# Performance work log

Measured on AMD Instinct MI355X. Metric: run time of the kernel, lower is better.

The kernel has to match this reference:

```python
import jax, jax.numpy as jnp
import numpy as np

D_MODEL = 1024
N_HEADS = 8
D_HEAD = 128
N_EXPERTS = 8
MOE_K = 2
SHARED = 1
ROUTED_E = N_EXPERTS - SHARED            # experts eligible for top-k routing
ROUTED_K = max(1, MOE_K - SHARED)        # routed slots per (token, head)
B, S = 4, 2048


def setup_inputs() -> dict:
    key = jax.random.key(0)
    ks = jax.random.split(key, 9)
    s = 1.0 / np.sqrt(D_MODEL)
    return {
        'q_src': jax.random.normal(ks[0], (B, S, D_MODEL), jnp.float32),
        'k_src': jax.random.normal(ks[1], (B, S, D_MODEL), jnp.float32),
        'v_src': jax.random.normal(ks[2], (B, S, D_MODEL), jnp.float32),
        'Wq': jax.random.normal(ks[3], (N_HEADS * D_HEAD, D_MODEL), jnp.float32) * s,
        'Wk': jax.random.normal(ks[4], (N_HEADS * D_HEAD, D_MODEL), jnp.float32) * s,
        'V': jax.random.normal(ks[5], (N_HEADS * N_EXPERTS, D_MODEL, D_HEAD), jnp.float32) * s,
        'O': jax.random.normal(ks[6], (N_HEADS * N_EXPERTS, D_HEAD, D_MODEL), jnp.float32) * (1.0 / np.sqrt(N_HEADS * D_HEAD)),
        'sel_v': jax.random.normal(ks[7], (N_HEADS * N_EXPERTS, D_MODEL), jnp.float32) * s,
        'sel_o': jax.random.normal(ks[8], (N_HEADS * N_EXPERTS, D_MODEL), jnp.float32) * s,
    }


def _gate(x, sel_w):
    # x: [B,S,D] -> sparse sigmoid gate [B,S,H,E] (eval mode: no expert dropout,
    # bias_v/bias_o are zeros so they do not change the top-k in the original).
    logits = jnp.einsum('bsd,ed->bse', x, sel_w)
    g = jax.nn.sigmoid(logits.astype(jnp.float32)).reshape(x.shape[0], x.shape[1], N_HEADS, N_EXPERTS)
    _, idx = jax.lax.top_k(g[..., :ROUTED_E], ROUTED_K)              # [B,S,H,Kr]
    shared = jnp.broadcast_to(jnp.arange(ROUTED_E, N_EXPERTS), idx.shape[:-1] + (SHARED,))
    idx = jnp.concatenate([idx, shared], axis=-1)                     # [B,S,H,K]
    vals = jnp.take_along_axis(g, idx, axis=-1)                       # sigmoid gate values
    onehot = jax.nn.one_hot(idx, N_EXPERTS, dtype=g.dtype)            # [B,S,H,K,E]
    return jnp.einsum('bshk,bshke->bshe', vals, onehot)               # sparse dense gate


def reference(q_src, k_src, v_src, Wq, Wk, V, O, sel_v, sel_o):
    scale_sqrt = jnp.asarray(D_HEAD, jnp.float32) ** -0.25  # sqrt(1/sqrt(d_head)), applied to q AND k
    b, s, _ = q_src.shape
    q = (q_src @ Wq.T * scale_sqrt).reshape(b, s, N_HEADS, D_HEAD).transpose(0, 2, 1, 3)  # [B,H,S,Dh]
    k = (k_src @ Wk.T * scale_sqrt).reshape(b, s, N_HEADS, D_HEAD).transpose(0, 2, 1, 3)

    gv = _gate(k_src, sel_v)   # value-expert gate, computed from k_src
    go = _gate(q_src, sel_o)   # output-expert gate, computed from q_src

    Vw = V.reshape(N_HEADS, N_EXPERTS, D_MODEL, D_HEAD)
    Ow = O.reshape(N_HEADS, N_EXPERTS, D_HEAD, D_MODEL)

    # CVMM value projection: per (token, head) mixture of expert V matrices
    v = jnp.einsum('bsd,hedf,bshe->bhsf', v_src, Vw, gv)              # [B,H,S,Dh]

    # SDPA, scale already folded into q and k; mask=None path
    attn = jax.nn.softmax(jnp.einsum('bhqf,bhkf->bhqk', q, k), axis=-1)
    res = jnp.einsum('bhqk,bhkf->bqhf', attn, v)                      # [B,S,H,Dh]

    # CVMM output projection: per (token, head) mixture of expert O matrices, summed over heads
    out = jnp.einsum('bqhf,hefd,bqhe->bqd', res, Ow, go)              # [B,S,D]
    return out
```

## Files before the change

kernel.cpp:

```cpp
#include <hip/hip_runtime.h>
#include <hip/hip_bf16.h>
#include <math.h>

#define BB 4
#define SS 2048
#define DM 1024
#define NH 8
#define DH 128
#define NE 8
#define NTOK (BB*SS)
#define SCALE_SQRT 0.29730177875068026f

typedef unsigned short u16;
typedef short s8v __attribute__((ext_vector_type(8)));
typedef float f4v __attribute__((ext_vector_type(4)));
#define MFMA16(a,b,c) __builtin_amdgcn_mfma_f32_16x16x32_bf16((a),(b),(c),0,0,0)

__device__ inline void bfsplit(float x, u16& h, u16& l) {
    unsigned u = __float_as_uint(x);
    unsigned hr = (u + 0x7FFFu + ((u >> 16) & 1u)) >> 16;
    h = (u16)hr;
    float hf = __uint_as_float(hr << 16);
    unsigned u2 = __float_as_uint(x - hf);
    l = (u16)((u2 + 0x7FFFu + ((u2 >> 16) & 1u)) >> 16);
}
__device__ inline u16 bf16rne(float x) {
    unsigned u = __float_as_uint(x);
    return (u16)((u + 0x7FFFu + ((u >> 16) & 1u)) >> 16);
}

__device__ inline void gll16(const u16* g, u16* l) {
    __builtin_amdgcn_global_load_lds(
        (const __attribute__((address_space(1))) unsigned int*)g,
        (__attribute__((address_space(3))) unsigned int*)l,
        16, 0, 0);
}

__device__ inline int swzoff(int row, int kchunk) {
    return row * 64 + ((kchunk ^ (row & 7)) << 3);
}

__global__ __launch_bounds__(256, 2) void proj_mfma_kernel(
        const u16* __restrict__ Ah_g, const u16* __restrict__ Al_g,
        const u16* __restrict__ Bh_g, const u16* __restrict__ Bl_g,
        u16* __restrict__ out_h, u16* __restrict__ out_l, float scale) {
    const int i0 = blockIdx.x * 128;
    const int n0 = blockIdx.y * 128;
    __shared__ u16 Ah[128 * 64], Al[128 * 64], Bh[128 * 64], Bl[128 * 64];
    const int t = threadIdx.x;
    const int lane = t & 63, wave = t >> 6;
    const int wm = wave >> 1, wn = wave & 1;
    const int ln = lane & 15, qd = lane >> 4;
    const f4v z4 = {0.f, 0.f, 0.f, 0.f};

    f4v C[4][4];
#pragma unroll
    for (int fm = 0; fm < 4; ++fm)
#pragma unroll
        for (int fn = 0; fn < 4; ++fn) C[fm][fn] = z4;

    for (int kb = 0; kb < 16; ++kb) {
        __syncthreads();
        const int kbase = kb * 64;
#pragma unroll
        for (int p = 0; p < 4; ++p) {
            int chunk = p * 256 + t;
            int row = chunk >> 3;
            int cs  = ((chunk & 7) ^ (row & 7)) * 8;
            int ld  = (p * 256 + (t & 192)) * 8;
            size_t ga = (size_t)(i0 + row) * 1024 + kbase + cs;
            gll16(&Ah_g[ga], &Ah[ld]);
            gll16(&Al_g[ga], &Al[ld]);
            size_t gb = (size_t)(n0 + row) * 1024 + kbase + cs;
            gll16(&Bh_g[gb], &Bh[ld]);
            gll16(&Bl_g[gb], &Bl[ld]);
        }
        __syncthreads();
#pragma unroll
        for (int ks = 0; ks < 2; ++ks) {
            s8v ah[4], alv[4], bh[4], blv[4];
#pragma unroll
            for (int fm = 0; fm < 4; ++fm) {
                int o = swzoff(wm * 64 + fm * 16 + ln, ks * 4 + qd);
                ah[fm]  = *(const s8v*)&Ah[o];
                alv[fm] = *(const s8v*)&Al[o];
            }
#pragma unroll
            for (int fn = 0; fn < 4; ++fn) {
                int o = swzoff(wn * 64 + fn * 16 + ln, ks * 4 + qd);
                bh[fn]  = *(const s8v*)&Bh[o];
                blv[fn] = *(const s8v*)&Bl[o];
            }
#pragma unroll
            for (int fm = 0; fm < 4; ++fm)
#pragma unroll
                for (int fn = 0; fn < 4; ++fn) {
                    C[fm][fn] = MFMA16(ah[fm],  bh[fn],  C[fm][fn]);
                    C[fm][fn] = MFMA16(ah[fm],  blv[fn], C[fm][fn]);
                    C[fm][fn] = MFMA16(alv[fm], bh[fn],  C[fm][fn]);
                }
        }
    }
    const int h = n0 >> 7;
#pragma unroll
    for (int fm = 0; fm < 4; ++fm)
#pragma unroll
        for (int fn = 0; fn < 4; ++fn)
#pragma unroll
            for (int r = 0; r < 4; ++r) {
                int token = i0 + wm * 64 + fm * 16 + qd * 4 + r;
                int f = wn * 64 + fn * 16 + ln;
                int b = token >> 11, s = token & 2047;
                u16 hh, ll;
                bfsplit(C[fm][fn][r] * scale, hh, ll);
                size_t o = ((((size_t)(b * NH + h)) * SS + s) << 7) + f;
                out_h[o] = hh; out_l[o] = ll;
            }
}

__global__ void gate_kernel(const float* __restrict__ x,
                            const float* __restrict__ sel,
                            float* __restrict__ gdense) {
    __shared__ float xs[DM];
    __shared__ float logits[64];
    __shared__ int   sbest[NH];
    __shared__ float sg1[NH], sg2[NH];
    const int token = blockIdx.x;
    const int t = threadIdx.x;
    const float* xp = x + (size_t)token * DM;
    for (int i = t; i < DM; i += 64) xs[i] = xp[i];
    __syncthreads();
    const float* sp = sel + (size_t)t * DM;
    float acc = 0.f;
    for (int d = 0; d < DM; ++d) acc += xs[d] * sp[d];
    logits[t] = acc;
    __syncthreads();
    if (t < NH) {
        const float* lp = logits + t * NE;
        int best = 0; float bv = lp[0];
#pragma unroll
        for (int e = 1; e < NE - 1; ++e)
            if (lp[e] > bv) { bv = lp[e]; best = e; }
        sbest[t] = best;
        sg1[t] = 1.f / (1.f + expf(-bv));
        sg2[t] = 1.f / (1.f + expf(-lp[NE - 1]));
    }
    __syncthreads();
    const int h = t >> 3, e = t & 7;
    float val = (e == sbest[h]) ? sg1[h] : ((e == NE - 1) ? sg2[h] : 0.f);
    gdense[(size_t)token * 64 + t] = val;
}

__global__ void split_kernel(const float* __restrict__ src,
                             u16* __restrict__ dh, u16* __restrict__ dl) {
    int i = (blockIdx.x * 256 + threadIdx.x) * 4;
    float4 v = *(const float4*)(src + i);
    u16 h[4], l[4];
    bfsplit(v.x, h[0], l[0]); bfsplit(v.y, h[1], l[1]);
    bfsplit(v.z, h[2], l[2]); bfsplit(v.w, h[3], l[3]);
    uint2 ph = { (unsigned)h[0] | ((unsigned)h[1] << 16),
                 (unsigned)h[2] | ((unsigned)h[3] << 16) };
    uint2 pl = { (unsigned)l[0] | ((unsigned)l[1] << 16),
                 (unsigned)l[2] | ((unsigned)l[3] << 16) };
    *(uint2*)&dh[i] = ph;
    *(uint2*)&dl[i] = pl;
}

__global__ void tsplit_kernel(const float* __restrict__ src,
                              u16* __restrict__ dh, u16* __restrict__ dl,
                              int R, int C) {
    __shared__ float tile[32][33];
    const int mat = blockIdx.x;
    const int r0 = blockIdx.y * 32, c0 = blockIdx.z * 32;
    const size_t base = (size_t)mat * R * C;
    const int tr = threadIdx.x >> 5, tc = threadIdx.x & 31;
#pragma unroll
    for (int p = 0; p < 4; ++p)
        tile[tr + p * 8][tc] = src[base + (size_t)(r0 + tr + p * 8) * C + c0 + tc];
    __syncthreads();
#pragma unroll
    for (int p = 0; p < 4; ++p) {
        int cc = tr + p * 8, rr = tc;
        float x = tile[rr][cc];
        u16 hh, ll; bfsplit(x, hh, ll);
        size_t o = base + (size_t)(c0 + cc) * R + r0 + rr;
        dh[o] = hh; dl[o] = ll;
    }
}

__global__ __launch_bounds__(256, 2) void v_mfma_kernel(
        const u16* __restrict__ Ah_g, const u16* __restrict__ Al_g,
        const u16* __restrict__ Bh_g, const u16* __restrict__ Bl_g,
        const float* __restrict__ gdense,
        float* __restrict__ wv) {
    const int i0 = blockIdx.x * 128;
    const int h  = blockIdx.y;
    __shared__ u16 Ah[128 * 64], Al[128 * 64], Bh[128 * 64], Bl[128 * 64];
    __shared__ float gl[128 * 8];
    const int t = threadIdx.x;
    const int lane = t & 63, wave = t >> 6;
    const int wm = wave >> 1, wn = wave & 1;
    const int ln = lane & 15, qd = lane >> 4;
    const f4v z4 = {0.f, 0.f, 0.f, 0.f};

#pragma unroll
    for (int p = 0; p < 4; ++p) {
        int idx = p * 256 + t;
        gl[idx] = gdense[(size_t)(i0 + (idx >> 3)) * 64 + h * 8 + (idx & 7)];
    }

    f4v C[4][4];
#pragma unroll
    for (int fm = 0; fm < 4; ++fm)
#pragma unroll
        for (int fn = 0; fn < 4; ++fn) C[fm][fn] = z4;

    for (int e = 0; e < 8; ++e) {
        f4v T[4][4];
#pragma unroll
        for (int fm = 0; fm < 4; ++fm)
#pragma unroll
            for (int fn = 0; fn < 4; ++fn) T[fm][fn] = z4;
        const size_t bbase = (size_t)(h * 8 + e) * DH * 1024;
        for (int kb = 0; kb < 16; ++kb) {
            __syncthreads();
            const int kbase = kb * 64;
#pragma unroll
            for (int p = 0; p < 4; ++p) {
                int chunk = p * 256 + t;
                int row = chunk >> 3;
                int cs  = ((chunk & 7) ^ (row & 7)) * 8;
                int ld  = (p * 256 + (t & 192)) * 8;
                size_t ga = (size_t)(i0 + row) * 1024 + kbase + cs;
                gll16(&Ah_g[ga], &Ah[ld]);
                gll16(&Al_g[ga], &Al[ld]);
                size_t gb = bbase + (size_t)row * 1024 + kbase + cs;
                gll16(&Bh_g[gb], &Bh[ld]);
                gll16(&Bl_g[gb], &Bl[ld]);
            }
            __syncthreads();
#pragma unroll
            for (int ks = 0; ks < 2; ++ks) {
                s8v ah[4], alv[4], bh[4], blv[4];
#pragma unroll
                for (int fm = 0; fm < 4; ++fm) {
                    int o = swzoff(wm * 64 + fm * 16 + ln, ks * 4 + qd);
                    ah[fm]  = *(const s8v*)&Ah[o];
                    alv[fm] = *(const s8v*)&Al[o];
                }
#pragma unroll
                for (int fn = 0; fn < 4; ++fn) {
                    int o = swzoff(wn * 64 + fn * 16 + ln, ks * 4 + qd);
                    bh[fn]  = *(const s8v*)&Bh[o];
                    blv[fn] = *(const s8v*)&Bl[o];
                }
#pragma unroll
                for (int fm = 0; fm < 4; ++fm)
#pragma unroll
                    for (int fn = 0; fn < 4; ++fn) {
                        T[fm][fn] = MFMA16(ah[fm],  bh[fn],  T[fm][fn]);
                        T[fm][fn] = MFMA16(ah[fm],  blv[fn], T[fm][fn]);
                        T[fm][fn] = MFMA16(alv[fm], bh[fn],  T[fm][fn]);
                    }
            }
        }
#pragma unroll
        for (int fm = 0; fm < 4; ++fm)
#pragma unroll
            for (int r = 0; r < 4; ++r) {
                float g = gl[(wm * 64 + fm * 16 + qd * 4 + r) * 8 + e];
#pragma unroll
                for (int fn = 0; fn < 4; ++fn)
                    C[fm][fn][r] += g * T[fm][fn][r];
            }
    }
#pragma unroll
    for (int fm = 0; fm < 4; ++fm)
#pragma unroll
        for (int fn = 0; fn < 4; ++fn)
#pragma unroll
            for (int r = 0; r < 4; ++r) {
                int token = i0 + wm * 64 + fm * 16 + qd * 4 + r;
                int f = wn * 64 + fn * 16 + ln;
                int b = token >> 11, s = token & 2047;
                wv[(((size_t)(b * NH + h) * SS + s) << 7) + f] = C[fm][fn][r];
            }
}

__global__ __launch_bounds__(256, 2) void out_mfma_kernel(
        const u16* __restrict__ Ah_g, const u16* __restrict__ Al_g,
        const u16* __restrict__ Bh_g, const u16* __restrict__ Bl_g,
        const float* __restrict__ gdense,
        float* __restrict__ out) {
    const int n0 = blockIdx.x * 128;
    const int i0 = blockIdx.y * 128;
    __shared__ u16 Ah[128 * 64], Al[128 * 64], Bh[128 * 64], Bl[128 * 64];
    __shared__ float gl[128 * 8];
    const int t = threadIdx.x;
    const int lane = t & 63, wave = t >> 6;
    const int wm = wave >> 1, wn = wave & 1;
    const int ln = lane & 15, qd = lane >> 4;
    const f4v z4 = {0.f, 0.f, 0.f, 0.f};

    f4v C[4][4];
#pragma unroll
    for (int fm = 0; fm < 4; ++fm)
#pragma unroll
        for (int fn = 0; fn < 4; ++fn) C[fm][fn] = z4;

    for (int h = 0; h < 8; ++h) {
        __syncthreads();
#pragma unroll
        for (int p = 0; p < 4; ++p) {
            int idx = p * 256 + t;
            gl[idx] = gdense[(size_t)(i0 + (idx >> 3)) * 64 + h * 8 + (idx & 7)];
        }
        for (int e = 0; e < 8; ++e) {
            f4v T[4][4];
#pragma unroll
            for (int fm = 0; fm < 4; ++fm)
#pragma unroll
                for (int fn = 0; fn < 4; ++fn) T[fm][fn] = z4;
            const size_t bbase = ((size_t)(h * 8 + e) * 1024 + n0) * DH;
#pragma unroll
            for (int kb = 0; kb < 2; ++kb) {
                __syncthreads();
                const int ka = h * 128 + kb * 64;
                const int kbb = kb * 64;
#pragma unroll
                for (int p = 0; p < 4; ++p) {
                    int chunk = p * 256 + t;
                    int row = chunk >> 3;
                    int cs  = ((chunk & 7) ^ (row & 7)) * 8;
                    int ld  = (p * 256 + (t & 192)) * 8;
                    size_t ga = (size_t)(i0 + row) * 1024 + ka + cs;
                    gll16(&Ah_g[ga], &Ah[ld]);
                    gll16(&Al_g[ga], &Al[ld]);
                    size_t gb = bbase + (size_t)row * DH + kbb + cs;
                    gll16(&Bh_g[gb], &Bh[ld]);
                    gll16(&Bl_g[gb], &Bl[ld]);
                }
                __syncthreads();
#pragma unroll
                for (int ks = 0; ks < 2; ++ks) {
                    s8v ah[4], alv[4], bh[4], blv[4];
#pragma unroll
                    for (int fm = 0; fm < 4; ++fm) {
                        int o = swzoff(wm * 64 + fm * 16 + ln, ks * 4 + qd);
                        ah[fm]  = *(const s8v*)&Ah[o];
                        alv[fm] = *(const s8v*)&Al[o];
                    }
#pragma unroll
                    for (int fn = 0; fn < 4; ++fn) {
                        int o = swzoff(wn * 64 + fn * 16 + ln, ks * 4 + qd);
                        bh[fn]  = *(const s8v*)&Bh[o];
                        blv[fn] = *(const s8v*)&Bl[o];
                    }
#pragma unroll
                    for (int fm = 0; fm < 4; ++fm)
#pragma unroll
                        for (int fn = 0; fn < 4; ++fn) {
                            T[fm][fn] = MFMA16(ah[fm],  bh[fn],  T[fm][fn]);
                            T[fm][fn] = MFMA16(ah[fm],  blv[fn], T[fm][fn]);
                            T[fm][fn] = MFMA16(alv[fm], bh[fn],  T[fm][fn]);
                        }
                }
            }
#pragma unroll
            for (int fm = 0; fm < 4; ++fm)
#pragma unroll
                for (int r = 0; r < 4; ++r) {
                    float g = gl[(wm * 64 + fm * 16 + qd * 4 + r) * 8 + e];
#pragma unroll
                    for (int fn = 0; fn < 4; ++fn)
                        C[fm][fn][r] += g * T[fm][fn][r];
                }
        }
    }
#pragma unroll
    for (int fm = 0; fm < 4; ++fm)
#pragma unroll
        for (int fn = 0; fn < 4; ++fn)
#pragma unroll
            for (int r = 0; r < 4; ++r) {
                int token = i0 + wm * 64 + fm * 16 + qd * 4 + r;
                int d = n0 + wn * 64 + fn * 16 + ln;
                out[(size_t)token * DM + d] = C[fm][fn][r];
            }
}

__global__ __launch_bounds__(256, 2) void attn_mfma_kernel(
        const u16* __restrict__ qh, const u16* __restrict__ ql,
        const u16* __restrict__ kh, const u16* __restrict__ kl,
        const u16* __restrict__ vth, const u16* __restrict__ vtl,
        u16* __restrict__ res_hi, u16* __restrict__ res_lo) {
    const int bid = blockIdx.x;
    const int bh = bid >> 4;
    const int q0 = (bid & 15) * 128;

    __shared__ u16 Ksh[32 * 136];
    __shared__ u16 Ksl[32 * 136];
    __shared__ u16 Vsh[128 * 40];
    __shared__ u16 Vsl[128 * 40];
    __shared__ u16 Ps[4][32 * 40];

    const int t = threadIdx.x;
    const int lane = t & 63, w = t >> 6;
    const int ln = lane & 15, qd = lane >> 4;

    s8v Qh[2][4], Qlv[2][4];
#pragma unroll
    for (int fm = 0; fm < 2; ++fm) {
        const size_t qoff = ((size_t)bh * SS + q0 + w * 32 + fm * 16 + ln) * DH;
        const u16* qhp = qh + qoff;
        const u16* qlp = ql + qoff;
#pragma unroll
        for (int ks = 0; ks < 4; ++ks) {
            Qh[fm][ks]  = *(const s8v*)(qhp + ks * 32 + qd * 8);
            Qlv[fm][ks] = *(const s8v*)(qlp + ks * 32 + qd * 8);
        }
    }

    f4v Of[2][8];
    const f4v z4 = {0.f, 0.f, 0.f, 0.f};
#pragma unroll
    for (int fm = 0; fm < 2; ++fm)
#pragma unroll
        for (int fn = 0; fn < 8; ++fn) Of[fm][fn] = z4;
    float mrow[2][4], lrow[2][4];
#pragma unroll
    for (int fm = 0; fm < 2; ++fm)
#pragma unroll
        for (int r = 0; r < 4; ++r) { mrow[fm][r] = -INFINITY; lrow[fm][r] = 0.f; }

    const u16* kbh = kh + (size_t)bh * SS * DH;
    const u16* kbl = kl + (size_t)bh * SS * DH;
    const u16* vbh = vth + (size_t)bh * DH * SS;
    const u16* vbl = vtl + (size_t)bh * DH * SS;

    const int krow0 = t >> 4,        kc0 = t & 15;
    const int krow1 = (256 + t) >> 4, kc1 = (256 + t) & 15;
    const int vrow0 = t >> 2,        vc0 = t & 3;
    const int vrow1 = (256 + t) >> 2, vc1 = (256 + t) & 3;
    const int kld0 = krow0 * 136 + kc0 * 8, kld1 = krow1 * 136 + kc1 * 8;
    const int vld0 = vrow0 * 40 + vc0 * 8,  vld1 = vrow1 * 40 + vc1 * 8;

    uint4 rKh0, rKh1, rKl0, rKl1, rVh0, rVh1, rVl0, rVl1;

#define LOADREGS(KT)                                                         \
    {                                                                        \
        size_t g0 = (size_t)((KT) * 32 + krow0) * DH + kc0 * 8;              \
        size_t g1 = (size_t)((KT) * 32 + krow1) * DH + kc1 * 8;              \
        rKh0 = *(const uint4*)&kbh[g0];  rKl0 = *(const uint4*)&kbl[g0];     \
        rKh1 = *(const uint4*)&kbh[g1];  rKl1 = *(const uint4*)&kbl[g1];     \
        size_t v0 = (size_t)vrow0 * SS + (KT) * 32 + vc0 * 8;                \
        size_t v1 = (size_t)vrow1 * SS + (KT) * 32 + vc1 * 8;                \
        rVh0 = *(const uint4*)&vbh[v0];  rVl0 = *(const uint4*)&vbl[v0];     \
        rVh1 = *(const uint4*)&vbh[v1];  rVl1 = *(const uint4*)&vbl[v1];     \
    }

#define STORELDS()                                                           \
    {                                                                        \
        *(uint4*)&Ksh[kld0] = rKh0;  *(uint4*)&Ksl[kld0] = rKl0;             \
        *(uint4*)&Ksh[kld1] = rKh1;  *(uint4*)&Ksl[kld1] = rKl1;             \
        *(uint4*)&Vsh[vld0] = rVh0;  *(uint4*)&Vsl[vld0] = rVl0;             \
        *(uint4*)&Vsh[vld1] = rVh1;  *(uint4*)&Vsl[vld1] = rVl1;             \
    }

    LOADREGS(0);
    STORELDS();
    __syncthreads();

    for (int kt = 0; kt < SS / 32; ++kt) {
        const bool more = (kt + 1 < SS / 32);
        if (more) LOADREGS(kt + 1);

        f4v S[2][2];
#pragma unroll
        for (int fm = 0; fm < 2; ++fm)
#pragma unroll
            for (int nt = 0; nt < 2; ++nt) S[fm][nt] = z4;
#pragma unroll
        for (int ks = 0; ks < 4; ++ks) {
#pragma unroll
            for (int nt = 0; nt < 2; ++nt) {
                int o = (nt * 16 + ln) * 136 + ks * 32 + qd * 8;
                s8v kbhf = *(const s8v*)&Ksh[o];
                s8v kblf = *(const s8v*)&Ksl[o];
#pragma unroll
                for (int fm = 0; fm < 2; ++fm) {
                    S[fm][nt] = MFMA16(Qh[fm][ks],  kbhf, S[fm][nt]);
                    S[fm][nt] = MFMA16(Qh[fm][ks],  kblf, S[fm][nt]);
                    S[fm][nt] = MFMA16(Qlv[fm][ks], kbhf, S[fm][nt]);
                }
            }
        }

        float pv[2][2][4];
#pragma unroll
        for (int fm = 0; fm < 2; ++fm) {
            float mt[4];
#pragma unroll
            for (int r = 0; r < 4; ++r) mt[r] = fmaxf(S[fm][0][r], S[fm][1][r]);
#pragma unroll
            for (int mask = 1; mask < 16; mask <<= 1)
#pragma unroll
                for (int r = 0; r < 4; ++r)
                    mt[r] = fmaxf(mt[r], __shfl_xor(mt[r], mask, 64));
            float alpha[4];
#pragma unroll
            for (int r = 0; r < 4; ++r) {
                float mn = fmaxf(mrow[fm][r], mt[r]);
                alpha[r] = __expf(mrow[fm][r] - mn);
                mrow[fm][r] = mn;
            }
            float lt[4] = {0.f, 0.f, 0.f, 0.f};
#pragma unroll
            for (int nt = 0; nt < 2; ++nt)
#pragma unroll
                for (int r = 0; r < 4; ++r) {
                    float p = __expf(S[fm][nt][r] - mrow[fm][r]);
                    pv[fm][nt][r] = p;
                    lt[r] += p;
                }
#pragma unroll
            for (int mask = 1; mask < 16; mask <<= 1)
#pragma unroll
                for (int r = 0; r < 4; ++r)
                    lt[r] += __shfl_xor(lt[r], mask, 64);
#pragma unroll
            for (int r = 0; r < 4; ++r)
                lrow[fm][r] = alpha[r] * lrow[fm][r] + lt[r];
#pragma unroll
            for (int fn = 0; fn < 8; ++fn)
#pragma unroll
                for (int r = 0; r < 4; ++r) Of[fm][fn][r] *= alpha[r];
        }

#pragma unroll
        for (int fm = 0; fm < 2; ++fm)
#pragma unroll
            for (int nt = 0; nt < 2; ++nt)
#pragma unroll
                for (int r = 0; r < 4; ++r)
                    Ps[w][(fm * 16 + qd * 4 + r) * 40 + nt * 16 + ln] =
                        bf16rne(pv[fm][nt][r]);

        s8v pf[2];
#pragma unroll
        for (int fm = 0; fm < 2; ++fm)
            pf[fm] = *(const s8v*)&Ps[w][(fm * 16 + ln) * 40 + qd * 8];
#pragma unroll
        for (int fn = 0; fn < 8; ++fn) {
            int o = (fn * 16 + ln) * 40 + qd * 8;
            s8v vbhf = *(const s8v*)&Vsh[o];
            s8v vblf = *(const s8v*)&Vsl[o];
#pragma unroll
            for (int fm = 0; fm < 2; ++fm) {
                Of[fm][fn] = MFMA16(pf[fm], vbhf, Of[fm][fn]);
                Of[fm][fn] = MFMA16(pf[fm], vblf, Of[fm][fn]);
            }
        }

        __syncthreads();
        if (more) {
            STORELDS();
            __syncthreads();
        }
    }

    const int b = bh >> 3, h = bh & 7;
#pragma unroll
    for (int fm = 0; fm < 2; ++fm)
#pragma unroll
        for (int r = 0; r < 4; ++r) {
            float linv = 1.f / lrow[fm][r];
            int qi = q0 + w * 32 + fm * 16 + qd * 4 + r;
            size_t off = (size_t)(b * SS + qi) * DM + h * DH + ln;
#pragma unroll
            for (int fn = 0; fn < 8; ++fn) {
                u16 hh, ll;
                bfsplit(Of[fm][fn][r] * linv, hh, ll);
                res_hi[off + fn * 16] = hh;
                res_lo[off + fn * 16] = ll;
            }
        }
#undef LOADREGS
#undef STORELDS
}

extern "C" void kernel_launch(void* const* d_in, const int* in_sizes, int n_in,
                              void* d_out, int out_size, void* d_ws, size_t ws_size,
                              hipStream_t stream) {
    (void)in_sizes; (void)n_in; (void)out_size; (void)ws_size;
    const float* q_src = (const float*)d_in[0];
    const float* k_src = (const float*)d_in[1];
    const float* v_src = (const float*)d_in[2];
    const float* Wq    = (const float*)d_in[3];
    const float* Wk    = (const float*)d_in[4];
    const float* V     = (const float*)d_in[5];
    const float* O     = (const float*)d_in[6];
    const float* sel_v = (const float*)d_in[7];
    const float* sel_o = (const float*)d_in[8];
    float* out = (float*)d_out;

    const size_t NELT = (size_t)NTOK * DM;
    u16* wq_h = (u16*)d_ws;
    u16* wq_l = wq_h + NELT;
    u16* wk_h = wq_l + NELT;
    u16* wk_l = wk_h + NELT;
    float* wv = (float*)(wk_l + NELT);
    u16* res_hi = (u16*)(wv + NELT);
    u16* res_lo = res_hi + NELT;
    u16* vs_hi  = res_lo + NELT;
    u16* vs_lo  = vs_hi + NELT;
    u16* Vt_hi  = vs_lo + NELT;
    u16* Vt_lo  = Vt_hi + NELT;
    float* gv = (float*)(Vt_lo + NELT);
    float* go = gv + (size_t)NTOK * 64;
    u16* Wq_h = (u16*)(go + (size_t)NTOK * 64);
    u16* Wq_l = Wq_h + (size_t)DM * DM;
    u16* Wk_h = Wq_l + (size_t)DM * DM;
    u16* Wk_l = Wk_h + (size_t)DM * DM;
    u16* qsrc_h = res_hi;
    u16* qsrc_l = res_lo;
    u16* ksrc_h = (u16*)wv;
    u16* ksrc_l = ksrc_h + NELT;
    u16* Ot_hi = vs_hi;
    u16* Ot_lo = vs_lo;
    u16* vth   = Vt_hi;
    u16* vtl   = Vt_lo;

    split_kernel<<<NELT / 1024, 256, 0, stream>>>(v_src, vs_hi, vs_lo);
    split_kernel<<<NELT / 1024, 256, 0, stream>>>(q_src, qsrc_h, qsrc_l);
    split_kernel<<<NELT / 1024, 256, 0, stream>>>(k_src, ksrc_h, ksrc_l);
    split_kernel<<<(DM * DM) / 1024, 256, 0, stream>>>(Wq, Wq_h, Wq_l);
    split_kernel<<<(DM * DM) / 1024, 256, 0, stream>>>(Wk, Wk_h, Wk_l);
    tsplit_kernel<<<dim3(64, 32, 4), 256, 0, stream>>>(V, Vt_hi, Vt_lo, 1024, 128);

    gate_kernel<<<NTOK, 64, 0, stream>>>(k_src, sel_v, gv);
    gate_kernel<<<NTOK, 64, 0, stream>>>(q_src, sel_o, go);

    proj_mfma_kernel<<<dim3(64, 8), 256, 0, stream>>>(
        qsrc_h, qsrc_l, Wq_h, Wq_l, wq_h, wq_l, SCALE_SQRT);
    proj_mfma_kernel<<<dim3(64, 8), 256, 0, stream>>>(
        ksrc_h, ksrc_l, Wk_h, Wk_l, wk_h, wk_l, SCALE_SQRT);

    v_mfma_kernel<<<dim3(64, 8), 256, 0, stream>>>(vs_hi, vs_lo, Vt_hi, Vt_lo, gv, wv);

    tsplit_kernel<<<dim3(64, 4, 32), 256, 0, stream>>>(O, Ot_hi, Ot_lo, 128, 1024);

    tsplit_kernel<<<dim3(32, 64, 4), 256, 0, stream>>>(wv, vth, vtl, 2048, 128);

    attn_mfma_kernel<<<BB * NH * (SS / 128), 256, 0, stream>>>(
        wq_h, wq_l, wk_h, wk_l, vth, vtl, res_hi, res_lo);

    out_mfma_kernel<<<dim3(8, 64), 256, 0, stream>>>(res_hi, res_lo, Ot_hi, Ot_lo, go, out);
}
```

Before: 1.702 ms.

## Route value-expert GEMM by bucketed tokens instead of dense over all experts

The gate kernel now records, for each (head, routed expert) bucket, the list of tokens that selected it and their gate values, using atomic counters. The value projection is split into a dense kernel for the always-on shared expert and a gathered grouped GEMM over each bucket's tokens. This removes the dense compute over all 8 experts, most of which had zero gate weight. It adds atomics, a gather-based A load, and a second read-modify-write of wv for the routed contribution. The gate kernel's loads are also vectorised to float4.

```diff
diff --git a/kernel.cpp b/kernel.cpp
--- a/kernel.cpp
+++ b/kernel.cpp
@@ -118,21 +118,34 @@
             }
 }
 
+__global__ void zero_kernel(int* __restrict__ p, int n) {
+    int i = blockIdx.x * 128 + threadIdx.x;
+    if (i < n) p[i] = 0;
+}
+
 __global__ void gate_kernel(const float* __restrict__ x,
                             const float* __restrict__ sel,
-                            float* __restrict__ gdense) {
+                            float* __restrict__ gdense,
+                            int* __restrict__ bcnt,
+                            int* __restrict__ bidx,
+                            float* __restrict__ bgv) {
     __shared__ float xs[DM];
     __shared__ float logits[64];
     __shared__ int   sbest[NH];
     __shared__ float sg1[NH], sg2[NH];
     const int token = blockIdx.x;
     const int t = threadIdx.x;
-    const float* xp = x + (size_t)token * DM;
-    for (int i = t; i < DM; i += 64) xs[i] = xp[i];
+    const float4* xp4 = (const float4*)(x + (size_t)token * DM);
+    float4* xs4 = (float4*)xs;
+    for (int i = t; i < DM / 4; i += 64) xs4[i] = xp4[i];
     __syncthreads();
-    const float* sp = sel + (size_t)t * DM;
+    const float4* sp4 = (const float4*)(sel + (size_t)t * DM);
     float acc = 0.f;
-    for (int d = 0; d < DM; ++d) acc += xs[d] * sp[d];
+    for (int d = 0; d < DM / 4; ++d) {
+        float4 a = xs4[d], b = sp4[d];
+        acc += a.x * b.x; acc += a.y * b.y;
+        acc += a.z * b.z; acc += a.w * b.w;
+    }
     logits[t] = acc;
     __syncthreads();
     if (t < NH) {
@@ -141,9 +154,16 @@
 #pragma unroll
         for (int e = 1; e < NE - 1; ++e)
             if (lp[e] > bv) { bv = lp[e]; best = e; }
+        float g1 = 1.f / (1.f + expf(-bv));
         sbest[t] = best;
-        sg1[t] = 1.f / (1.f + expf(-bv));
+        sg1[t] = g1;
         sg2[t] = 1.f / (1.f + expf(-lp[NE - 1]));
+        if (bidx != nullptr) {
+            int bk = t * 7 + best;
+            int slot = atomicAdd(&bcnt[bk], 1);
+            bidx[(size_t)bk * NTOK + slot] = token;
+            bgv [(size_t)bk * NTOK + slot] = g1;
+        }
     }
     __syncthreads();
     const int h = t >> 3, e = t & 7;
@@ -188,7 +208,7 @@
     }
 }
 
-__global__ __launch_bounds__(256, 2) void v_mfma_kernel(
+__global__ __launch_bounds__(256, 2) void v_shared_kernel(
         const u16* __restrict__ Ah_g, const u16* __restrict__ Al_g,
         const u16* __restrict__ Bh_g, const u16* __restrict__ Bl_g,
         const float* __restrict__ gdense,
@@ -196,18 +216,14 @@
     const int i0 = blockIdx.x * 128;
     const int h  = blockIdx.y;
     __shared__ u16 Ah[128 * 64], Al[128 * 64], Bh[128 * 64], Bl[128 * 64];
-    __shared__ float gl[128 * 8];
+    __shared__ float gl[128];
     const int t = threadIdx.x;
     const int lane = t & 63, wave = t >> 6;
     const int wm = wave >> 1, wn = wave & 1;
     const int ln = lane & 15, qd = lane >> 4;
     const f4v z4 = {0.f, 0.f, 0.f, 0.f};
 
-#pragma unroll
-    for (int p = 0; p < 4; ++p) {
-        int idx = p * 256 + t;
-        gl[idx] = gdense[(size_t)(i0 + (idx >> 3)) * 64 + h * 8 + (idx & 7)];
-    }
+    if (t < 128) gl[t] = gdense[(size_t)(i0 + t) * 64 + h * 8 + 7];
 
     f4v C[4][4];
 #pragma unroll
@@ -215,75 +231,156 @@
 #pragma unroll
         for (int fn = 0; fn < 4; ++fn) C[fm][fn] = z4;
 
-    for (int e = 0; e < 8; ++e) {
-        f4v T[4][4];
-#pragma unroll
-        for (int fm = 0; fm < 4; ++fm)
-#pragma unroll
-            for (int fn = 0; fn < 4; ++fn) T[fm][fn] = z4;
-        const size_t bbase = (size_t)(h * 8 + e) * DH * 1024;
-        for (int kb = 0; kb < 16; ++kb) {
-            __syncthreads();
-            const int kbase = kb * 64;
-#pragma unroll
-            for (int p = 0; p < 4; ++p) {
-                int chunk = p * 256 + t;
-                int row = chunk >> 3;
-                int cs  = ((chunk & 7) ^ (row & 7)) * 8;
-                int ld  = (p * 256 + (t & 192)) * 8;
-                size_t ga = (size_t)(i0 + row) * 1024 + kbase + cs;
-                gll16(&Ah_g[ga], &Ah[ld]);
-                gll16(&Al_g[ga], &Al[ld]);
-                size_t gb = bbase + (size_t)row * 1024 + kbase + cs;
-                gll16(&Bh_g[gb], &Bh[ld]);
-                gll16(&Bl_g[gb], &Bl[ld]);
-            }
-            __syncthreads();
-#pragma unroll
-            for (int ks = 0; ks < 2; ++ks) {
-                s8v ah[4], alv[4], bh[4], blv[4];
-#pragma unroll
-                for (int fm = 0; fm < 4; ++fm) {
-                    int o = swzoff(wm * 64 + fm * 16 + ln, ks * 4 + qd);
-                    ah[fm]  = *(const s8v*)&Ah[o];
-                    alv[fm] = *(const s8v*)&Al[o];
+    const size_t bbase = (size_t)(h * 8 + 7) * DH * 1024;
+    for (int kb = 0; kb < 16; ++kb) {
+        __syncthreads();
+        const int kbase = kb * 64;
+#pragma unroll
+        for (int p = 0; p < 4; ++p) {
+            int chunk = p * 256 + t;
+            int row = chunk >> 3;
+            int cs  = ((chunk & 7) ^ (row & 7)) * 8;
+            int ld  = (p * 256 + (t & 192)) * 8;
+            size_t ga = (size_t)(i0 + row) * 1024 + kbase + cs;
+            gll16(&Ah_g[ga], &Ah[ld]);
+            gll16(&Al_g[ga], &Al[ld]);
+            size_t gb = bbase + (size_t)row * 1024 + kbase + cs;
+            gll16(&Bh_g[gb], &Bh[ld]);
+            gll16(&Bl_g[gb], &Bl[ld]);
+        }
+        __syncthreads();
+#pragma unroll
+        for (int ks = 0; ks < 2; ++ks) {
+            s8v ah[4], alv[4], bh[4], blv[4];
+#pragma unroll
+            for (int fm = 0; fm < 4; ++fm) {
+                int o = swzoff(wm * 64 + fm * 16 + ln, ks * 4 + qd);
+                ah[fm]  = *(const s8v*)&Ah[o];
+                alv[fm] = *(const s8v*)&Al[o];
+            }
+#pragma unroll
+            for (int fn = 0; fn < 4; ++fn) {
+                int o = swzoff(wn * 64 + fn * 16 + ln, ks * 4 + qd);
+                bh[fn]  = *(const s8v*)&Bh[o];
+                blv[fn] = *(const s8v*)&Bl[o];
+            }
+#pragma unroll
+            for (int fm = 0; fm < 4; ++fm)
+#pragma unroll
+                for (int fn = 0; fn < 4; ++fn) {
+                    C[fm][fn] = MFMA16(ah[fm],  bh[fn],  C[fm][fn]);
+                    C[fm][fn] = MFMA16(ah[fm],  blv[fn], C[fm][fn]);
+                    C[fm][fn] = MFMA16(alv[fm], bh[fn],  C[fm][fn]);
                 }
-#pragma unroll
-                for (int fn = 0; fn < 4; ++fn) {
-                    int o = swzoff(wn * 64 + fn * 16 + ln, ks * 4 + qd);
-                    bh[fn]  = *(const s8v*)&Bh[o];
-                    blv[fn] = *(const s8v*)&Bl[o];
-                }
-#pragma unroll
-                for (int fm = 0; fm < 4; ++fm)
-#pragma unroll
-                    for (int fn = 0; fn < 4; ++fn) {
-                        T[fm][fn] = MFMA16(ah[fm],  bh[fn],  T[fm][fn]);
-                        T[fm][fn] = MFMA16(ah[fm],  blv[fn], T[fm][fn]);
-                        T[fm][fn] = MFMA16(alv[fm], bh[fn],  T[fm][fn]);
-                    }
-            }
-        }
-#pragma unroll
-        for (int fm = 0; fm < 4; ++fm)
+        }
+    }
+#pragma unroll
+    for (int fm = 0; fm < 4; ++fm)
+#pragma unroll
+        for (int fn = 0; fn < 4; ++fn)
 #pragma unroll
             for (int r = 0; r < 4; ++r) {
-                float g = gl[(wm * 64 + fm * 16 + qd * 4 + r) * 8 + e];
-#pragma unroll
-                for (int fn = 0; fn < 4; ++fn)
-                    C[fm][fn][r] += g * T[fm][fn][r];
-            }
-    }
-#pragma unroll
-    for (int fm = 0; fm < 4; ++fm)
-#pragma unroll
-        for (int fn = 0; fn < 4; ++fn)
-#pragma unroll
-            for (int r = 0; r < 4; ++r) {
-                int token = i0 + wm * 64 + fm * 16 + qd * 4 + r;
+                int row = wm * 64 + fm * 16 + qd * 4 + r;
+                int token = i0 + row;
                 int f = wn * 64 + fn * 16 + ln;
                 int b = token >> 11, s = token & 2047;
-                wv[(((size_t)(b * NH + h) * SS + s) << 7) + f] = C[fm][fn][r];
+                wv[(((size_t)(b * NH + h) * SS + s) << 7) + f] = gl[row] * C[fm][fn][r];
+            }
+}
+
+__global__ __launch_bounds__(256, 2) void v_routed_kernel(
+        const u16* __restrict__ Ah_g, const u16* __restrict__ Al_g,
+        const u16* __restrict__ Bh_g, const u16* __restrict__ Bl_g,
+        const int* __restrict__ bcnt, const int* __restrict__ bidx,
+        const float* __restrict__ bgv,
+        float* __restrict__ wv) {
+    const int bucket = blockIdx.y;
+    const int cnt = bcnt[bucket];
+    const int tile0 = blockIdx.x * 128;
+    if (tile0 >= cnt) return;
+    const int h = bucket / 7, e = bucket % 7;
+    const int rows = min(128, cnt - tile0);
+    __shared__ u16 Ah[128 * 64], Al[128 * 64], Bh[128 * 64], Bl[128 * 64];
+    __shared__ int   toks[128];
+    __shared__ float gvals[128];
+    const int t = threadIdx.x;
+    const int lane = t & 63, wave = t >> 6;
+    const int wm = wave >> 1, wn = wave & 1;
+    const int ln = lane & 15, qd = lane >> 4;
+    const f4v z4 = {0.f, 0.f, 0.f, 0.f};
+
+    if (t < 128) {
+        int slot = tile0 + min(t, rows - 1);
+        toks[t]  = bidx[(size_t)bucket * NTOK + slot];
+        gvals[t] = bgv [(size_t)bucket * NTOK + slot];
+    }
+    __syncthreads();
+    const int rb = t >> 3;
+    const int tok0 = toks[rb], tok1 = toks[32 + rb];
+    const int tok2 = toks[64 + rb], tok3 = toks[96 + rb];
+
+    f4v C[4][4];
+#pragma unroll
+    for (int fm = 0; fm < 4; ++fm)
+#pragma unroll
+        for (int fn = 0; fn < 4; ++fn) C[fm][fn] = z4;
+
+    const size_t bbase = (size_t)(h * 8 + e) * DH * 1024;
+    for (int kb = 0; kb < 16; ++kb) {
+        __syncthreads();
+        const int kbase = kb * 64;
+#pragma unroll
+        for (int p = 0; p < 4; ++p) {
+            int chunk = p * 256 + t;
+            int row = chunk >> 3;
+            int cs  = ((chunk & 7) ^ (row & 7)) * 8;
+            int ld  = (p * 256 + (t & 192)) * 8;
+            int tok = (p == 0) ? tok0 : (p == 1) ? tok1 : (p == 2) ? tok2 : tok3;
+            size_t ga = (size_t)tok * 1024 + kbase + cs;
+            gll16(&Ah_g[ga], &Ah[ld]);
+            gll16(&Al_g[ga], &Al[ld]);
+            size_t gb = bbase + (size_t)row * 1024 + kbase + cs;
+            gll16(&Bh_g[gb], &Bh[ld]);
+            gll16(&Bl_g[gb], &Bl[ld]);
+        }
+        __syncthreads();
+#pragma unroll
+        for (int ks = 0; ks < 2; ++ks) {
+            s8v ah[4], alv[4], bh[4], blv[4];
+#pragma unroll
+            for (int fm = 0; fm < 4; ++fm) {
+                int o = swzoff(wm * 64 + fm * 16 + ln, ks * 4 + qd);
+                ah[fm]  = *(const s8v*)&Ah[o];
+                alv[fm] = *(const s8v*)&Al[o];
+            }
+#pragma unroll
+            for (int fn = 0; fn < 4; ++fn) {
+                int o = swzoff(wn * 64 + fn * 16 + ln, ks * 4 + qd);
+                bh[fn]  = *(const s8v*)&Bh[o];
+                blv[fn] = *(const s8v*)&Bl[o];
+            }
+#pragma unroll
+            for (int fm = 0; fm < 4; ++fm)
+#pragma unroll
+                for (int fn = 0; fn < 4; ++fn) {
+                    C[fm][fn] = MFMA16(ah[fm],  bh[fn],  C[fm][fn]);
+                    C[fm][fn] = MFMA16(ah[fm],  blv[fn], C[fm][fn]);
+                    C[fm][fn] = MFMA16(alv[fm], bh[fn],  C[fm][fn]);
+                }
+        }
+    }
+#pragma unroll
+    for (int fm = 0; fm < 4; ++fm)
+#pragma unroll
+        for (int fn = 0; fn < 4; ++fn)
+#pragma unroll
+            for (int r = 0; r < 4; ++r) {
+                int row = wm * 64 + fm * 16 + qd * 4 + r;
+                if (row >= rows) continue;
+                int token = toks[row];
+                int f = wn * 64 + fn * 16 + ln;
+                int b = token >> 11, s = token & 2047;
+                wv[(((size_t)(b * NH + h) * SS + s) << 7) + f] += gvals[row] * C[fm][fn][r];
             }
 }
 
@@ -622,6 +719,9 @@
     u16* Wq_l = Wq_h + (size_t)DM * DM;
     u16* Wk_h = Wq_l + (size_t)DM * DM;
     u16* Wk_l = Wk_h + (size_t)DM * DM;
+    int* bcnt_v = (int*)(Wk_l + (size_t)DM * DM);
+    int* bidx_v = bcnt_v + 64;
+    float* bgv_v = (float*)(bidx_v + (size_t)56 * NTOK);
     u16* qsrc_h = res_hi;
     u16* qsrc_l = res_lo;
     u16* ksrc_h = (u16*)wv;
@@ -638,15 +738,18 @@
     split_kernel<<<(DM * DM) / 1024, 256, 0, stream>>>(Wk, Wk_h, Wk_l);
     tsplit_kernel<<<dim3(64, 32, 4), 256, 0, stream>>>(V, Vt_hi, Vt_lo, 1024, 128);
 
-    gate_kernel<<<NTOK, 64, 0, stream>>>(k_src, sel_v, gv);
-    gate_kernel<<<NTOK, 64, 0, stream>>>(q_src, sel_o, go);
+    zero_kernel<<<1, 128, 0, stream>>>(bcnt_v, 56);
+    gate_kernel<<<NTOK, 64, 0, stream>>>(k_src, sel_v, gv, bcnt_v, bidx_v, bgv_v);
+    gate_kernel<<<NTOK, 64, 0, stream>>>(q_src, sel_o, go, nullptr, nullptr, nullptr);
 
     proj_mfma_kernel<<<dim3(64, 8), 256, 0, stream>>>(
         qsrc_h, qsrc_l, Wq_h, Wq_l, wq_h, wq_l, SCALE_SQRT);
     proj_mfma_kernel<<<dim3(64, 8), 256, 0, stream>>>(
         ksrc_h, ksrc_l, Wk_h, Wk_l, wk_h, wk_l, SCALE_SQRT);
 
-    v_mfma_kernel<<<dim3(64, 8), 256, 0, stream>>>(vs_hi, vs_lo, Vt_hi, Vt_lo, gv, wv);
+    v_shared_kernel<<<dim3(64, 8), 256, 0, stream>>>(vs_hi, vs_lo, Vt_hi, Vt_lo, gv, wv);
+    v_routed_kernel<<<dim3(64, 56), 256, 0, stream>>>(vs_hi, vs_lo, Vt_hi, Vt_lo,
+                                                      bcnt_v, bidx_v, bgv_v, wv);
 
     tsplit_kernel<<<dim3(64, 4, 32), 256, 0, stream>>>(O, Ot_hi, Ot_lo, 128, 1024);
 
```

New measurement: 1.693 ms. No clear change (-0.5%).
